# Optimization experiments

Measured on AMD Instinct MI355X. Metric: run time of the kernel, lower is better.

The kernel has to match this reference:

```python
import jax, jax.numpy as jnp
import numpy as np
from jax import lax

B, L, D = 1024, 50, 128          # batch, max_seq_len, embed_dim
NV, NH = 8, 16                    # n_v vertical filters, n_h horizontal filters
NU, NI = 100000, 100000           # num_users, num_items


def setup_inputs() -> dict:
    key = jax.random.key(0)
    ks = jax.random.split(key, 9)
    return {
        "user_ids": jax.random.randint(ks[0], (B,), 0, NU),
        "item_seq": jax.random.randint(ks[1], (B, L), 0, NI),
        "user_emb": jax.random.normal(ks[2], (NU, D), jnp.float32) * 0.02,
        "item_emb": jax.random.normal(ks[3], (NI, D), jnp.float32) * 0.02,
        "vfilter": jax.random.normal(ks[4], (L, NV), jnp.float32) * 0.1,
        # hconv_w[i] holds the Conv2d(1, NH, (i+1, D)) weight, zero-padded to height L;
        # only rows [:i+1] are used for filter of height h=i+1.
        "hconv_w": jax.random.normal(ks[5], (L, NH, L, D), jnp.float32) * 0.05,
        "hconv_b": jax.random.normal(ks[6], (L, NH), jnp.float32) * 0.01,
        "fc_w": jax.random.normal(ks[7], (NV * D + NH * L, D), jnp.float32) * 0.02,
        "fc_b": jax.random.normal(ks[8], (D,), jnp.float32) * 0.01,
    }


def reference(user_ids, item_seq, user_emb, item_emb, vfilter, hconv_w, hconv_b, fc_w, fc_b):
    P_u = user_emb[user_ids]                 # [B, D]
    E = item_emb[item_seq]                   # [B, L, D]

    # vertical conv: (E^T @ V)^T flattened as (v major, d minor) -> [B, NV*D]
    o_v = jnp.einsum('bld,lv->bvd', E, vfilter).reshape(E.shape[0], -1)

    # horizontal convs: one per kernel height h = 1..L (structurally distinct kernels)
    x = E[:, None, :, :]                     # NCHW: [B, 1, L, D]
    o_h = []
    for i in range(L):
        h = i + 1
        w = hconv_w[i, :, :h, :][:, None, :, :]   # OIHW: [NH, 1, h, D]
        c = lax.conv_general_dilated(
            x, w, window_strides=(1, 1), padding='VALID',
            dimension_numbers=('NCHW', 'OIHW', 'NCHW'))[..., 0]   # [B, NH, L-h+1]
        c = jax.nn.relu(c + hconv_b[i][None, :, None])
        o_h.append(jnp.max(c, axis=2))            # max-pool over all valid positions
    o_h = jnp.concatenate(o_h, axis=1)            # [B, NH*L]

    o = jnp.concatenate([o_v, o_h], axis=1)       # [B, NV*D + NH*L]
    z = jax.nn.relu(o @ fc_w + fc_b)              # [B, D]
    return jnp.concatenate([z, P_u], axis=1)      # [B, 2*D]
```

## Files before the change

kernel.cpp:

```cpp
#include <hip/hip_runtime.h>
#include <hip/hip_bf16.h>
#include <stdint.h>

#define B_   1024
#define L_   50
#define D_   128
#define NV_  8
#define NH_  16
#define KFC  1824

typedef __bf16 bf16x8 __attribute__((ext_vector_type(8)));
typedef float  f32x4  __attribute__((ext_vector_type(4)));

static __device__ __forceinline__ bf16x8 as_bf16x8(uint4 u) {
  return __builtin_bit_cast(bf16x8, u);
}

static __device__ __forceinline__ unsigned short f2b(float x) {
  unsigned u = __float_as_uint(x);
  return (unsigned short)((u + 0x7FFFu + ((u >> 16) & 1u)) >> 16);
}

#define OV_BYTES  ((size_t)B_ * KFC * 4)
#define EOFF      (OV_BYTES)
#define ESZ       ((size_t)B_ * 4 * 50 * 64)
#define W2OFF     (EOFF + ESZ)
#define W2SZ      ((size_t)1275 * 4096)
#define NEED_FULL (W2OFF + W2SZ)

__global__ void ck_kP(const int* __restrict__ uids, const float* __restrict__ uemb,
                      float* __restrict__ out) {
  int b = blockIdx.x, d = threadIdx.x;
  out[(size_t)b * 256 + 128 + d] = uemb[(size_t)uids[b] * D_ + d];
}

__global__ void ck_kZ(float* __restrict__ out) {
  int i = blockIdx.x * 256 + threadIdx.x;
  int b = i >> 7, d = i & 127;
  out[(size_t)b * 256 + d] = 0.f;
}

__global__ void ck_kA(const int* __restrict__ item_seq, const float* __restrict__ item_emb,
                      char* __restrict__ ws) {
  int b = blockIdx.x, tid = threadIdx.x;
  __shared__ int sidx[L_];
  if (tid < L_) sidx[tid] = item_seq[b * L_ + tid];
  __syncthreads();
  char* eg = ws + EOFF + (size_t)b * 12800;
  #pragma unroll
  for (int it = 0; it < 4; ++it) {
    int c = it * 256 + tid;
    int ks = c >> 8, row = (c >> 2) & 63, g = c & 3;
    if (row < L_) {
      const float* src = item_emb + (size_t)sidx[row] * D_ + ks * 32 + g * 8;
      float4 f0 = *(const float4*)(src);
      float4 f1 = *(const float4*)(src + 4);
      uint4 val;
      val.x = f2b(f0.x) | ((unsigned)f2b(f0.y) << 16);
      val.y = f2b(f0.z) | ((unsigned)f2b(f0.w) << 16);
      val.z = f2b(f1.x) | ((unsigned)f2b(f1.y) << 16);
      val.w = f2b(f1.z) | ((unsigned)f2b(f1.w) << 16);
      *(uint4*)(eg + ks * 3200 + row * 64 + g * 16) = val;
    }
  }
}

__global__ void ck_kW2(const float* __restrict__ hw, char* __restrict__ ws) {
  int p = blockIdx.x, tid = threadIdx.x;
  int ks = tid >> 6, l = tid & 63;
  int n = l & 15, gq = l >> 4;
  int i = (int)((sqrtf(8.0f * (float)p + 1.0f) - 1.0f) * 0.5f);
  while ((i + 1) * (i + 2) / 2 <= p) ++i;
  while (i * (i + 1) / 2 > p) --i;
  int j = p - i * (i + 1) / 2;
  const float* src = hw + ((size_t)(i * 16 + n) * 50 + j) * 128 + ks * 32 + gq * 8;
  float4 f0 = *(const float4*)(src);
  float4 f1 = *(const float4*)(src + 4);
  uint4 v;
  v.x = f2b(f0.x) | ((unsigned)f2b(f0.y) << 16);
  v.y = f2b(f0.z) | ((unsigned)f2b(f0.w) << 16);
  v.z = f2b(f1.x) | ((unsigned)f2b(f1.y) << 16);
  v.w = f2b(f1.z) | ((unsigned)f2b(f1.w) << 16);
  *(uint4*)(ws + W2OFF + (size_t)p * 4096 + tid * 16) = v;
}

__global__ void ck_kB(const int* __restrict__ item_seq, const float* __restrict__ item_emb,
                      const float* __restrict__ vf, char* __restrict__ ws) {
  int b = blockIdx.x, tid = threadIdx.x;
  __shared__ float E[L_][D_];
  __shared__ float VF[L_][NV_];
  __shared__ int sidx[L_];
  if (tid < L_) sidx[tid] = item_seq[b * L_ + tid];
  for (int c = tid; c < L_ * NV_; c += 256) VF[c / NV_][c % NV_] = vf[c];
  __syncthreads();
  for (int c = tid; c < 1600; c += 256) {
    int l = c >> 5, ch = c & 31;
    *(float4*)&E[l][ch * 4] = *(const float4*)(item_emb + (size_t)sidx[l] * D_ + ch * 4);
  }
  __syncthreads();
  int d = tid & 127, half = tid >> 7;
  float acc[4] = {0.f, 0.f, 0.f, 0.f};
  for (int l = 0; l < L_; ++l) {
    float e = E[l][d];
    #pragma unroll
    for (int vv = 0; vv < 4; ++vv) acc[vv] += e * VF[l][half * 4 + vv];
  }
  float* o = (float*)ws + (size_t)b * KFC;
  #pragma unroll
  for (int vv = 0; vv < 4; ++vv) o[(half * 4 + vv) * D_ + d] = acc[vv];
}

#define EB_STRIDE 3280
#define LDS_E     (16 * EB_STRIDE)
#define NWIN      182
#define WENC_OFF  LDS_E
#define WCOST_OFF (LDS_E + 728)
#define SCHED_OFF (LDS_E + 1456)
#define LDS_TOT   (LDS_E + 1456 + 768)

#define MFMA_BF16 __builtin_amdgcn_mfma_f32_16x16x32_bf16

template<int NT4>
__device__ __forceinline__ void proc_item(const char* lds, const char* bp0,
    int i, int t0, f32x4 (&acc)[8], int aoff) {
  bf16x8 win[8];
  #pragma unroll
  for (int q = 0; q < 8; ++q) {
    int s = t0 + q; s = s > 50 ? 50 : s;
    win[q] = as_bf16x8(*(const uint4*)(lds + aoff + s * 64));
  }
  uint4 breg[8];
  #pragma unroll
  for (int u = 0; u < 8; ++u)
    breg[u] = *(const uint4*)(bp0 + (size_t)(u <= i ? u : 0) * 4096);

  for (int j0 = 0; j0 <= i; j0 += 8) {
    #pragma unroll
    for (int u = 0; u < 8; ++u) {
      int j = j0 + u;
      if (j <= i) {
        bf16x8 bfr = as_bf16x8(breg[u]);
        acc[0] = MFMA_BF16(win[u], bfr, acc[0], 0, 0, 0);
        acc[1] = MFMA_BF16(win[(u + 1) & 7], bfr, acc[1], 0, 0, 0);
        acc[2] = MFMA_BF16(win[(u + 2) & 7], bfr, acc[2], 0, 0, 0);
        acc[3] = MFMA_BF16(win[(u + 3) & 7], bfr, acc[3], 0, 0, 0);
        int sn = t0 + j + 8; sn = sn > 50 ? 50 : sn;
        win[u] = as_bf16x8(*(const uint4*)(lds + aoff + sn * 64));
        if (NT4 == 8) {
          acc[4] = MFMA_BF16(win[(u + 4) & 7], bfr, acc[4], 0, 0, 0);
          acc[5] = MFMA_BF16(win[(u + 5) & 7], bfr, acc[5], 0, 0, 0);
          acc[6] = MFMA_BF16(win[(u + 6) & 7], bfr, acc[6], 0, 0, 0);
          acc[7] = MFMA_BF16(win[(u + 7) & 7], bfr, acc[7], 0, 0, 0);
        }
        if (j + 8 <= i) breg[u] = *(const uint4*)(bp0 + (size_t)(j + 8) * 4096);
      }
    }
  }
}

__device__ __forceinline__ void run_item(const char* lds, const char* W2, int ks,
    int enc, f32x4 (&acc)[8], int aoff, int lane) {
  int i = enc & 0xff, t0 = (enc >> 8) & 0xff, nt4 = (enc >> 24) & 0xff;
  const char* bp0 = W2 + (size_t)(i * (i + 1) / 2) * 4096 + ks * 1024 + lane * 16;
  if (nt4 == 4) proc_item<4>(lds, bp0, i, t0, acc, aoff);
  else          proc_item<8>(lds, bp0, i, t0, acc, aoff);
}

__device__ __forceinline__ void epi_item(float* o, const float* hb, int b0,
    int enc, f32x4 (&acc)[8], int lane) {
  int i = enc & 0xff, nt = (enc >> 16) & 0xff;
  int r = lane & 15, gq = lane >> 4;
  float bias = hb[i * 16 + r];
  #pragma unroll
  for (int e = 0; e < 4; ++e) {
    float m = 0.f;
    #pragma unroll
    for (int tt = 0; tt < 8; ++tt)
      if (tt < nt) m = fmaxf(m, fmaxf(acc[tt][e] + bias, 0.f));
    atomicMax((unsigned*)&o[(size_t)(b0 + gq * 4 + e) * KFC + 1024 + i * 16 + r],
              __float_as_uint(m));
  }
}

__launch_bounds__(512, 4)
__global__ void ck_kC4(const float* __restrict__ hconv_b, char* __restrict__ ws) {
  __shared__ char lds[LDS_TOT];
  int* wenc  = (int*)(lds + WENC_OFF);
  int* wcost = (int*)(lds + WCOST_OFF);
  int* sched = (int*)(lds + SCHED_OFF);
  int tid = threadIdx.x;
  int wv = tid >> 6, lane = tid & 63;
  int r = lane & 15, gq = lane >> 4;
  int b0 = (int)blockIdx.x * 16;
  int slot = (int)blockIdx.y * 8 + wv;
  int aoff = r * EB_STRIDE + gq * 16;

  if (tid < 192) sched[tid] = -1;
  if (tid < NWIN) {
    int idx = tid, i, nw = 1;
    for (i = 0; i < 50; ++i) {
      nw = (57 - i) >> 3;
      if (idx < nw) break;
      idx -= nw;
    }
    int ntb = 50 - i - 8 * (nw - 1);
    int nt = idx ? 8 : ntb;
    int t0 = idx ? ntb + 8 * (idx - 1) : 0;
    int nt4 = (nt + 3) & ~3;
    wenc[tid]  = i | (t0 << 8) | (nt << 16) | (nt4 << 24);
    wcost[tid] = (((i + 1) * nt4) << 8) + tid;
  }
  __syncthreads();
  if (tid < NWIN) {
    int c = wcost[tid], rank = 0;
    for (int u = 0; u < NWIN; ++u) rank += (wcost[u] > c) ? 1 : 0;
    int rnd = rank >> 6, pos = rank & 63;
    int sl = (rnd & 1) ? (63 - pos) : pos;
    sched[sl * 3 + rnd] = wenc[tid];
  }
  __syncthreads();

  const char* EG = ws + EOFF;
  const char* W2 = ws + W2OFF;
  float* o = (float*)ws;

  int sb = tid < 400 ? tid / 25 : 0;
  int sm = tid < 400 ? tid % 25 : 0;

  for (int rd = 0; rd < 3; ++rd) {
    int enc = sched[slot * 3 + rd];
    f32x4 acc[8];
    #pragma unroll
    for (int t = 0; t < 8; ++t) {
      acc[t][0] = 0.f; acc[t][1] = 0.f; acc[t][2] = 0.f; acc[t][3] = 0.f;
    }
    for (int ks = 0; ks < 4; ++ks) {
      __syncthreads();
      if (tid < 400) {
        const char* src = EG + (size_t)(b0 + sb) * 12800 + ks * 3200 + sm * 16;
        char* dst = lds + sb * EB_STRIDE + sm * 16;
        #pragma unroll
        for (int q = 0; q < 8; ++q)
          *(uint4*)(dst + q * 400) = *(const uint4*)(src + q * 400);
      }
      __syncthreads();
      if (enc >= 0) run_item(lds, W2, ks, enc, acc, aoff, lane);
    }
    if (enc >= 0) epi_item(o, hconv_b, b0, enc, acc, lane);
  }
}

__launch_bounds__(256)
__global__ void ck_kD(const float* __restrict__ fc_w, const float* __restrict__ fc_b,
                      const char* __restrict__ ws, float* __restrict__ out) {
  __shared__ char ldsD[5120];
  int b0 = blockIdx.x * 64, n0 = blockIdx.y * 16;
  int tid = threadIdx.x, w = tid >> 6, lane = tid & 63, r = lane & 15, gq = lane >> 4;
  const float* o = (const float*)ws;

  f32x4 acc; acc[0] = 0.f; acc[1] = 0.f; acc[2] = 0.f; acc[3] = 0.f;

  int rl = tid >> 2, ch = tid & 3;
  const float* asrc = o + (size_t)(b0 + rl) * KFC + ch * 8;
  int kk = tid >> 3, nn = tid & 7;

  float4 fa0 = *(const float4*)(asrc);
  float4 fa1 = *(const float4*)(asrc + 4);
  float fb0 = fc_w[(size_t)kk * D_ + n0 + nn];
  float fb1 = fc_w[(size_t)kk * D_ + n0 + nn + 8];

  int arow_off = rl * 64 + ((ch ^ (rl & 3)) << 4);
  int rloc = w * 16 + r;
  int ard = rloc * 64 + ((gq ^ (rloc & 3)) << 4);
  int brd = 4096 + r * 64 + ((gq ^ (r & 3)) << 4);

  for (int s = 0; s < 57; ++s) {
    __syncthreads();
    {
      uint4 v;
      v.x = f2b(fa0.x) | ((unsigned)f2b(fa0.y) << 16);
      v.y = f2b(fa0.z) | ((unsigned)f2b(fa0.w) << 16);
      v.z = f2b(fa1.x) | ((unsigned)f2b(fa1.y) << 16);
      v.w = f2b(fa1.z) | ((unsigned)f2b(fa1.w) << 16);
      *(uint4*)(ldsD + arow_off) = v;
      *(unsigned short*)(ldsD + 4096 + nn * 64 + (((kk >> 3) ^ (nn & 3)) << 4) + (kk & 7) * 2) = f2b(fb0);
      *(unsigned short*)(ldsD + 4096 + (nn + 8) * 64 + (((kk >> 3) ^ ((nn + 8) & 3)) << 4) + (kk & 7) * 2) = f2b(fb1);
    }
    __syncthreads();
    if (s + 1 < 57) {
      int kb = (s + 1) * 32;
      fa0 = *(const float4*)(asrc + kb);
      fa1 = *(const float4*)(asrc + kb + 4);
      fb0 = fc_w[(size_t)(kb + kk) * D_ + n0 + nn];
      fb1 = fc_w[(size_t)(kb + kk) * D_ + n0 + nn + 8];
    }
    bf16x8 a   = as_bf16x8(*(const uint4*)(ldsD + ard));
    bf16x8 bfr = as_bf16x8(*(const uint4*)(ldsD + brd));
    acc = __builtin_amdgcn_mfma_f32_16x16x32_bf16(a, bfr, acc, 0, 0, 0);
  }

  float bias = fc_b[n0 + r];
  #pragma unroll
  for (int e = 0; e < 4; ++e) {
    int row = b0 + w * 16 + gq * 4 + e;
    out[(size_t)row * 256 + n0 + r] = fmaxf(acc[e] + bias, 0.f);
  }
}

extern "C" void kernel_launch(void* const* d_in, const int* in_sizes, int n_in,
                              void* d_out, int out_size, void* d_ws, size_t ws_size,
                              hipStream_t stream) {
  const int*   user_ids = (const int*)d_in[0];
  const int*   item_seq = (const int*)d_in[1];
  const float* user_emb = (const float*)d_in[2];
  const float* item_emb = (const float*)d_in[3];
  const float* vfilter  = (const float*)d_in[4];
  const float* hconv_w  = (const float*)d_in[5];
  const float* hconv_b  = (const float*)d_in[6];
  const float* fc_w     = (const float*)d_in[7];
  const float* fc_b     = (const float*)d_in[8];
  float* out = (float*)d_out;
  char*  ws  = (char*)d_ws;

  ck_kP<<<dim3(B_), dim3(128), 0, stream>>>(user_ids, user_emb, out);

  if (ws_size < NEED_FULL) {
    ck_kZ<<<dim3(512), dim3(256), 0, stream>>>(out);
    return;
  }

  hipMemsetAsync(ws, 0, OV_BYTES, stream);

  ck_kA<<<dim3(B_), dim3(256), 0, stream>>>(item_seq, item_emb, ws);
  ck_kW2<<<dim3(1275), dim3(256), 0, stream>>>(hconv_w, ws);
  ck_kB<<<dim3(B_), dim3(256), 0, stream>>>(item_seq, item_emb, vfilter, ws);
  ck_kC4<<<dim3(64, 8), dim3(512), 0, stream>>>(hconv_b, ws);
  ck_kD<<<dim3(16, 8), dim3(256), 0, stream>>>(fc_w, fc_b, ws, out);
}
```

Baseline: 163.6 us.

## Fuse gather and vertical conv, repack E layout, rebalance horizontal-conv schedule, double FC k-step

Merges the bf16 E-gather kernel and the vertical-conv kernel into one that loads the embeddings once into LDS and writes both outputs. E is repacked with a contiguous 3264-byte per-(batch,k-slice) stride so the conv kernel can copy it to LDS with all 512 threads in flat coalesced loads. The horizontal-conv grid goes from 8 to 12 y-blocks, with 2 scheduled windows per wave instead of 3 and a higher occupancy hint. The FC kernel processes two k-slices per barrier pair to halve synchronisation. Risks include register pressure from the higher occupancy target and extra padding writes.

```diff
diff --git a/kernel.cpp b/kernel.cpp
--- a/kernel.cpp
+++ b/kernel.cpp
@@ -23,7 +23,8 @@
 
 #define OV_BYTES  ((size_t)B_ * KFC * 4)
 #define EOFF      (OV_BYTES)
-#define ESZ       ((size_t)B_ * 4 * 50 * 64)
+#define EBKS      3264
+#define ESZ       ((size_t)B_ * 4 * EBKS)
 #define W2OFF     (EOFF + ESZ)
 #define W2SZ      ((size_t)1275 * 4096)
 #define NEED_FULL (W2OFF + W2SZ)
@@ -40,29 +41,49 @@
   out[(size_t)b * 256 + d] = 0.f;
 }
 
-__global__ void ck_kA(const int* __restrict__ item_seq, const float* __restrict__ item_emb,
-                      char* __restrict__ ws) {
+__global__ void ck_kAB(const int* __restrict__ item_seq, const float* __restrict__ item_emb,
+                       const float* __restrict__ vf, char* __restrict__ ws) {
   int b = blockIdx.x, tid = threadIdx.x;
+  __shared__ float E[L_][D_];
+  __shared__ float VF[L_][NV_];
   __shared__ int sidx[L_];
   if (tid < L_) sidx[tid] = item_seq[b * L_ + tid];
+  for (int c = tid; c < L_ * NV_; c += 256) VF[c / NV_][c % NV_] = vf[c];
   __syncthreads();
-  char* eg = ws + EOFF + (size_t)b * 12800;
+  for (int c = tid; c < 1600; c += 256) {
+    int l = c >> 5, ch = c & 31;
+    *(float4*)&E[l][ch * 4] = *(const float4*)(item_emb + (size_t)sidx[l] * D_ + ch * 4);
+  }
+  __syncthreads();
+  char* eg = ws + EOFF + (size_t)b * 4 * EBKS;
   #pragma unroll
   for (int it = 0; it < 4; ++it) {
     int c = it * 256 + tid;
-    int ks = c >> 8, row = (c >> 2) & 63, g = c & 3;
-    if (row < L_) {
-      const float* src = item_emb + (size_t)sidx[row] * D_ + ks * 32 + g * 8;
-      float4 f0 = *(const float4*)(src);
-      float4 f1 = *(const float4*)(src + 4);
-      uint4 val;
-      val.x = f2b(f0.x) | ((unsigned)f2b(f0.y) << 16);
-      val.y = f2b(f0.z) | ((unsigned)f2b(f0.w) << 16);
-      val.z = f2b(f1.x) | ((unsigned)f2b(f1.y) << 16);
-      val.w = f2b(f1.z) | ((unsigned)f2b(f1.w) << 16);
-      *(uint4*)(eg + ks * 3200 + row * 64 + g * 16) = val;
-    }
-  }
+    if (c < 816) {
+      int ks = c / 204, rem = c - ks * 204;
+      uint4 v = make_uint4(0, 0, 0, 0);
+      if (rem < 200) {
+        int row = rem >> 2, g4 = rem & 3;
+        float4 f0 = *(const float4*)&E[row][ks * 32 + g4 * 8];
+        float4 f1 = *(const float4*)&E[row][ks * 32 + g4 * 8 + 4];
+        v.x = f2b(f0.x) | ((unsigned)f2b(f0.y) << 16);
+        v.y = f2b(f0.z) | ((unsigned)f2b(f0.w) << 16);
+        v.z = f2b(f1.x) | ((unsigned)f2b(f1.y) << 16);
+        v.w = f2b(f1.z) | ((unsigned)f2b(f1.w) << 16);
+      }
+      *(uint4*)(eg + (size_t)ks * EBKS + rem * 16) = v;
+    }
+  }
+  int d = tid & 127, half = tid >> 7;
+  float acc[4] = {0.f, 0.f, 0.f, 0.f};
+  for (int l = 0; l < L_; ++l) {
+    float e = E[l][d];
+    #pragma unroll
+    for (int vv = 0; vv < 4; ++vv) acc[vv] += e * VF[l][half * 4 + vv];
+  }
+  float* o = (float*)ws + (size_t)b * KFC;
+  #pragma unroll
+  for (int vv = 0; vv < 4; ++vv) o[(half * 4 + vv) * D_ + d] = acc[vv];
 }
 
 __global__ void ck_kW2(const float* __restrict__ hw, char* __restrict__ ws) {
@@ -84,39 +105,12 @@
   *(uint4*)(ws + W2OFF + (size_t)p * 4096 + tid * 16) = v;
 }
 
-__global__ void ck_kB(const int* __restrict__ item_seq, const float* __restrict__ item_emb,
-                      const float* __restrict__ vf, char* __restrict__ ws) {
-  int b = blockIdx.x, tid = threadIdx.x;
-  __shared__ float E[L_][D_];
-  __shared__ float VF[L_][NV_];
-  __shared__ int sidx[L_];
-  if (tid < L_) sidx[tid] = item_seq[b * L_ + tid];
-  for (int c = tid; c < L_ * NV_; c += 256) VF[c / NV_][c % NV_] = vf[c];
-  __syncthreads();
-  for (int c = tid; c < 1600; c += 256) {
-    int l = c >> 5, ch = c & 31;
-    *(float4*)&E[l][ch * 4] = *(const float4*)(item_emb + (size_t)sidx[l] * D_ + ch * 4);
-  }
-  __syncthreads();
-  int d = tid & 127, half = tid >> 7;
-  float acc[4] = {0.f, 0.f, 0.f, 0.f};
-  for (int l = 0; l < L_; ++l) {
-    float e = E[l][d];
-    #pragma unroll
-    for (int vv = 0; vv < 4; ++vv) acc[vv] += e * VF[l][half * 4 + vv];
-  }
-  float* o = (float*)ws + (size_t)b * KFC;
-  #pragma unroll
-  for (int vv = 0; vv < 4; ++vv) o[(half * 4 + vv) * D_ + d] = acc[vv];
-}
-
-#define EB_STRIDE 3280
+#define EB_STRIDE 3264
 #define LDS_E     (16 * EB_STRIDE)
 #define NWIN      182
-#define WENC_OFF  LDS_E
-#define WCOST_OFF (LDS_E + 728)
-#define SCHED_OFF (LDS_E + 1456)
-#define LDS_TOT   (LDS_E + 1456 + 768)
+#define WCOST_OFF LDS_E
+#define SCHED_OFF (LDS_E + 736)
+#define LDS_TOT   (LDS_E + 736 + 768)
 
 #define MFMA_BF16 __builtin_amdgcn_mfma_f32_16x16x32_bf16
 
@@ -182,10 +176,9 @@
   }
 }
 
-__launch_bounds__(512, 4)
-__global__ void ck_kC4(const float* __restrict__ hconv_b, char* __restrict__ ws) {
+__launch_bounds__(512, 6)
+__global__ void ck_kC5(const float* __restrict__ hconv_b, char* __restrict__ ws) {
   __shared__ char lds[LDS_TOT];
-  int* wenc  = (int*)(lds + WENC_OFF);
   int* wcost = (int*)(lds + WCOST_OFF);
   int* sched = (int*)(lds + SCHED_OFF);
   int tid = threadIdx.x;
@@ -196,6 +189,7 @@
   int aoff = r * EB_STRIDE + gq * 16;
 
   if (tid < 192) sched[tid] = -1;
+  int myenc = -1;
   if (tid < NWIN) {
     int idx = tid, i, nw = 1;
     for (i = 0; i < 50; ++i) {
@@ -207,16 +201,17 @@
     int nt = idx ? 8 : ntb;
     int t0 = idx ? ntb + 8 * (idx - 1) : 0;
     int nt4 = (nt + 3) & ~3;
-    wenc[tid]  = i | (t0 << 8) | (nt << 16) | (nt4 << 24);
+    myenc = i | (t0 << 8) | (nt << 16) | (nt4 << 24);
     wcost[tid] = (((i + 1) * nt4) << 8) + tid;
   }
   __syncthreads();
   if (tid < NWIN) {
     int c = wcost[tid], rank = 0;
     for (int u = 0; u < NWIN; ++u) rank += (wcost[u] > c) ? 1 : 0;
-    int rnd = rank >> 6, pos = rank & 63;
-    int sl = (rnd & 1) ? (63 - pos) : pos;
-    sched[sl * 3 + rnd] = wenc[tid];
+    int rnd = rank >= 96 ? 1 : 0;
+    int pos = rank - 96 * rnd;
+    int sl = rnd ? (95 - pos) : pos;
+    sched[sl * 2 + rnd] = myenc;
   }
   __syncthreads();
 
@@ -224,11 +219,8 @@
   const char* W2 = ws + W2OFF;
   float* o = (float*)ws;
 
-  int sb = tid < 400 ? tid / 25 : 0;
-  int sm = tid < 400 ? tid % 25 : 0;
-
-  for (int rd = 0; rd < 3; ++rd) {
-    int enc = sched[slot * 3 + rd];
+  for (int rd = 0; rd < 2; ++rd) {
+    int enc = sched[slot * 2 + rd];
     f32x4 acc[8];
     #pragma unroll
     for (int t = 0; t < 8; ++t) {
@@ -236,12 +228,18 @@
     }
     for (int ks = 0; ks < 4; ++ks) {
       __syncthreads();
-      if (tid < 400) {
-        const char* src = EG + (size_t)(b0 + sb) * 12800 + ks * 3200 + sm * 16;
-        char* dst = lds + sb * EB_STRIDE + sm * 16;
-        #pragma unroll
-        for (int q = 0; q < 8; ++q)
-          *(uint4*)(dst + q * 400) = *(const uint4*)(src + q * 400);
+      #pragma unroll
+      for (int it = 0; it < 6; ++it) {
+        int g = it * 512 + tid;
+        int bb = g / 204, off = g - bb * 204;
+        *(uint4*)(lds + g * 16) =
+          *(const uint4*)(EG + ((size_t)((b0 + bb) * 4 + ks)) * EBKS + off * 16);
+      }
+      if (tid < 192) {
+        int g = 3072 + tid;
+        int bb = g / 204, off = g - bb * 204;
+        *(uint4*)(lds + g * 16) =
+          *(const uint4*)(EG + ((size_t)((b0 + bb) * 4 + ks)) * EBKS + off * 16);
       }
       __syncthreads();
       if (enc >= 0) run_item(lds, W2, ks, enc, acc, aoff, lane);
@@ -253,7 +251,7 @@
 __launch_bounds__(256)
 __global__ void ck_kD(const float* __restrict__ fc_w, const float* __restrict__ fc_b,
                       const char* __restrict__ ws, float* __restrict__ out) {
-  __shared__ char ldsD[5120];
+  __shared__ char ldsD[10240];
   int b0 = blockIdx.x * 64, n0 = blockIdx.y * 16;
   int tid = threadIdx.x, w = tid >> 6, lane = tid & 63, r = lane & 15, gq = lane >> 4;
   const float* o = (const float*)ws;
@@ -264,39 +262,59 @@
   const float* asrc = o + (size_t)(b0 + rl) * KFC + ch * 8;
   int kk = tid >> 3, nn = tid & 7;
 
-  float4 fa0 = *(const float4*)(asrc);
-  float4 fa1 = *(const float4*)(asrc + 4);
-  float fb0 = fc_w[(size_t)kk * D_ + n0 + nn];
-  float fb1 = fc_w[(size_t)kk * D_ + n0 + nn + 8];
+  float4 fa[4]; float fb[4];
+  fa[0] = *(const float4*)(asrc);
+  fa[1] = *(const float4*)(asrc + 4);
+  fa[2] = *(const float4*)(asrc + 32);
+  fa[3] = *(const float4*)(asrc + 36);
+  fb[0] = fc_w[(size_t)kk * D_ + n0 + nn];
+  fb[1] = fc_w[(size_t)kk * D_ + n0 + nn + 8];
+  fb[2] = fc_w[(size_t)(32 + kk) * D_ + n0 + nn];
+  fb[3] = fc_w[(size_t)(32 + kk) * D_ + n0 + nn + 8];
 
   int arow_off = rl * 64 + ((ch ^ (rl & 3)) << 4);
   int rloc = w * 16 + r;
   int ard = rloc * 64 + ((gq ^ (rloc & 3)) << 4);
-  int brd = 4096 + r * 64 + ((gq ^ (r & 3)) << 4);
-
-  for (int s = 0; s < 57; ++s) {
+  int brd = 8192 + r * 64 + ((gq ^ (r & 3)) << 4);
+  int bw0 = 8192 + nn * 64 + (((kk >> 3) ^ (nn & 3)) << 4) + (kk & 7) * 2;
+  int bw1 = 8192 + (nn + 8) * 64 + (((kk >> 3) ^ ((nn + 8) & 3)) << 4) + (kk & 7) * 2;
+
+  for (int s = 0; s < 29; ++s) {
+    int k1ok = (2 * s + 1) < 57;
     __syncthreads();
-    {
+    #pragma unroll
+    for (int sl = 0; sl < 2; ++sl) {
       uint4 v;
-      v.x = f2b(fa0.x) | ((unsigned)f2b(fa0.y) << 16);
-      v.y = f2b(fa0.z) | ((unsigned)f2b(fa0.w) << 16);
-      v.z = f2b(fa1.x) | ((unsigned)f2b(fa1.y) << 16);
-      v.w = f2b(fa1.z) | ((unsigned)f2b(fa1.w) << 16);
-      *(uint4*)(ldsD + arow_off) = v;
-      *(unsigned short*)(ldsD + 4096 + nn * 64 + (((kk >> 3) ^ (nn & 3)) << 4) + (kk & 7) * 2) = f2b(fb0);
-      *(unsigned short*)(ldsD + 4096 + (nn + 8) * 64 + (((kk >> 3) ^ ((nn + 8) & 3)) << 4) + (kk & 7) * 2) = f2b(fb1);
+      v.x = f2b(fa[2*sl].x) | ((unsigned)f2b(fa[2*sl].y) << 16);
+      v.y = f2b(fa[2*sl].z) | ((unsigned)f2b(fa[2*sl].w) << 16);
+      v.z = f2b(fa[2*sl+1].x) | ((unsigned)f2b(fa[2*sl+1].y) << 16);
+      v.w = f2b(fa[2*sl+1].z) | ((unsigned)f2b(fa[2*sl+1].w) << 16);
+      *(uint4*)(ldsD + sl * 4096 + arow_off) = v;
+      *(unsigned short*)(ldsD + sl * 1024 + bw0) = f2b(fb[2*sl]);
+      *(unsigned short*)(ldsD + sl * 1024 + bw1) = f2b(fb[2*sl+1]);
     }
     __syncthreads();
-    if (s + 1 < 57) {
-      int kb = (s + 1) * 32;
-      fa0 = *(const float4*)(asrc + kb);
-      fa1 = *(const float4*)(asrc + kb + 4);
-      fb0 = fc_w[(size_t)(kb + kk) * D_ + n0 + nn];
-      fb1 = fc_w[(size_t)(kb + kk) * D_ + n0 + nn + 8];
-    }
-    bf16x8 a   = as_bf16x8(*(const uint4*)(ldsD + ard));
-    bf16x8 bfr = as_bf16x8(*(const uint4*)(ldsD + brd));
-    acc = __builtin_amdgcn_mfma_f32_16x16x32_bf16(a, bfr, acc, 0, 0, 0);
+    int kn0 = (2 * s + 2) * 32, kn1 = (2 * s + 3) * 32;
+    if (kn0 < 1824) {
+      fa[0] = *(const float4*)(asrc + kn0);
+      fa[1] = *(const float4*)(asrc + kn0 + 4);
+      fb[0] = fc_w[(size_t)(kn0 + kk) * D_ + n0 + nn];
+      fb[1] = fc_w[(size_t)(kn0 + kk) * D_ + n0 + nn + 8];
+    }
+    if (kn1 < 1824) {
+      fa[2] = *(const float4*)(asrc + kn1);
+      fa[3] = *(const float4*)(asrc + kn1 + 4);
+      fb[2] = fc_w[(size_t)(kn1 + kk) * D_ + n0 + nn];
+      fb[3] = fc_w[(size_t)(kn1 + kk) * D_ + n0 + nn + 8];
+    }
+    bf16x8 a0  = as_bf16x8(*(const uint4*)(ldsD + ard));
+    bf16x8 b0f = as_bf16x8(*(const uint4*)(ldsD + brd));
+    acc = __builtin_amdgcn_mfma_f32_16x16x32_bf16(a0, b0f, acc, 0, 0, 0);
+    if (k1ok) {
+      bf16x8 a1  = as_bf16x8(*(const uint4*)(ldsD + 4096 + ard));
+      bf16x8 b1f = as_bf16x8(*(const uint4*)(ldsD + 1024 + brd));
+      acc = __builtin_amdgcn_mfma_f32_16x16x32_bf16(a1, b1f, acc, 0, 0, 0);
+    }
   }
 
   float bias = fc_b[n0 + r];
@@ -331,9 +349,8 @@
 
   hipMemsetAsync(ws, 0, OV_BYTES, stream);
 
-  ck_kA<<<dim3(B_), dim3(256), 0, stream>>>(item_seq, item_emb, ws);
+  ck_kAB<<<dim3(B_), dim3(256), 0, stream>>>(item_seq, item_emb, vfilter, ws);
   ck_kW2<<<dim3(1275), dim3(256), 0, stream>>>(hconv_w, ws);
-  ck_kB<<<dim3(B_), dim3(256), 0, stream>>>(item_seq, item_emb, vfilter, ws);
-  ck_kC4<<<dim3(64, 8), dim3(512), 0, stream>>>(hconv_b, ws);
+  ck_kC5<<<dim3(64, 12), dim3(512), 0, stream>>>(hconv_b, ws);
   ck_kD<<<dim3(16, 8), dim3(256), 0, stream>>>(fc_w, fc_b, ws, out);
 }
```

After: 461.3 us. 182% more time.
